# Kernel optimization log

Measured on AMD Instinct MI355X. Metric: run time of the kernel, lower is better.

The kernel has to match this reference:

```python
import jax, jax.numpy as jnp
import numpy as np

B, L, C = 8, 4096, 256
H = 8            # num_heads
D = C // H       # head_dim = 32
CHUNK = 128


def _build_slopes(n):
    # ALiBi slopes for power-of-2 n: 2^(-8/n * (i+1)); cast fp16 like the torch module
    s = np.array([2.0 ** (-(8.0 / n) * (i + 1)) for i in range(n)], dtype=np.float32)
    return jnp.asarray(s.astype(np.float16).astype(np.float32))  # [H]


def setup_inputs() -> dict:
    key = jax.random.key(0)
    ks = jax.random.split(key, 6)
    x = jax.random.normal(ks[0], (B, L, C), dtype=jnp.float32)
    rel_pos = jax.random.normal(ks[1], (1, L, C), dtype=jnp.float32) * 0.02  # trunc_normal std=0.02
    qkv_w = jax.random.normal(ks[2], (3 * C, C), dtype=jnp.float32) * (C ** -0.5)
    q_gamma = jnp.ones((H, 1, D), dtype=jnp.float32) / (D ** 0.5)
    k_gamma = jnp.ones((H, 1, D), dtype=jnp.float32) / (D ** 0.5)
    proj_w = jax.random.normal(ks[3], (C, C), dtype=jnp.float32) * (C ** -0.5)
    proj_b = jnp.zeros((C,), dtype=jnp.float32)
    return {"x": x, "rel_pos": rel_pos, "qkv_w": qkv_w, "q_gamma": q_gamma,
            "k_gamma": k_gamma, "proj_w": proj_w, "proj_b": proj_b}


def _rms_norm(t, gamma):
    # t: [B,H,L,D]; gamma: [H,1,D]. F.normalize(dim=-1) then * sqrt(D) * gamma
    n = jnp.sqrt(jnp.sum(t * t, axis=-1, keepdims=True))
    t = t / jnp.maximum(n, 1e-12)
    return t * (D ** 0.5) * gamma[None]


def _lightning_attn(q, k, v, slopes):
    # q,k,v: [B,H,L,D]; slopes: [H]. o_t = sum_{s<=t} exp(-slope*(t-s)) (q_t.k_s) v_s
    nc = L // CHUNK
    c = CHUNK
    qc = q.reshape(B, H, nc, c, D)
    kc = k.reshape(B, H, nc, c, D)
    vc = v.reshape(B, H, nc, c, D)

    idx = jnp.arange(c, dtype=jnp.float32)
    diff = idx[:, None] - idx[None, :]                       # [c,c]
    s = slopes[:, None, None]                                # [H,1,1]
    mask = jnp.where(diff >= 0, jnp.exp(-s * diff), 0.0)     # [H,c,c]

    # intra-chunk: [B,H,nc,c,c]
    scores = jnp.einsum("bhncd,bhnmd->bhncm", qc, kc) * mask[None, :, None]
    o_intra = jnp.einsum("bhncm,bhnmd->bhncd", scores, vc)

    # inter-chunk recurrence over decayed KV state [B,H,D,D]
    q_decay = jnp.exp(-slopes[:, None] * idx[None, :])[None, :, :, None]        # [1,H,c,1]
    k_decay = jnp.exp(-slopes[:, None] * (c - idx[None, :]))[None, :, :, None]  # [1,H,c,1]
    blk_decay = jnp.exp(-slopes * c)[:, None, None]                             # [H,1,1]

    def step(kv, inp):
        qi, ki, vi = inp                                   # each [B,H,c,D]
        o = jnp.einsum("bhcd,bhde->bhce", qi * q_decay, kv)
        kv = blk_decay * kv + jnp.einsum("bhcd,bhce->bhde", ki * k_decay, vi)
        return kv, o

    kv0 = jnp.zeros((B, H, D, D), dtype=q.dtype)
    qs = jnp.moveaxis(qc, 2, 0)  # [nc,B,H,c,D]
    ks_ = jnp.moveaxis(kc, 2, 0)
    vs = jnp.moveaxis(vc, 2, 0)
    _, o_inter = jax.lax.scan(step, kv0, (qs, ks_, vs))    # [nc,B,H,c,D]
    o_inter = jnp.moveaxis(o_inter, 0, 2)                  # [B,H,nc,c,D]

    return (o_intra + o_inter).reshape(B, H, L, D)


def reference(x, rel_pos, qkv_w, q_gamma, k_gamma, proj_w, proj_b):
    slopes = _build_slopes(H)
    h = x + rel_pos                                        # [B,L,C]
    qkv = h @ qkv_w.T                                      # [B,L,3C]
    qkv = qkv.reshape(B, L, 3, H, D).transpose(2, 0, 3, 1, 4)  # [3,B,H,L,D]
    q, k, v = qkv[0], qkv[1], qkv[2]
    q = q * (D ** -0.5)            # no-op through normalize, kept for fidelity
    q = _rms_norm(q, q_gamma)
    k = _rms_norm(k, k_gamma)
    o = _lightning_attn(q, k, v, slopes)                   # [B,H,L,D]
    o = o.transpose(0, 2, 1, 3).reshape(B, L, C)
    return o @ proj_w.T + proj_b
```

## Files before the change

kernel.cpp:

```cpp
#include <hip/hip_runtime.h>
#include <hip/hip_bf16.h>

#define B_ 8
#define L_ 4096
#define C_ 256
#define H_ 8
#define D_ 32
#define CHUNK_ 128
#define NC_ 32
#define M_ (B_*L_)

typedef _Float16 f16x8 __attribute__((ext_vector_type(8)));
typedef _Float16 f16x4 __attribute__((ext_vector_type(4)));
typedef float    f32x4 __attribute__((ext_vector_type(4)));

#define GLOAD_LDS16(g, l) __builtin_amdgcn_global_load_lds( \
    (const __attribute__((address_space(1))) unsigned int*)(g), \
    (__attribute__((address_space(3))) unsigned int*)(l), 16, 0, 0)

__global__ __launch_bounds__(256) void k_cast_h(
    const float* __restrict__ x, const float* __restrict__ rel, _Float16* __restrict__ h)
{
    const int i = (blockIdx.x * 256 + threadIdx.x) * 8;
    float4 x0 = *(const float4*)(x + i);
    float4 x1 = *(const float4*)(x + i + 4);
    const int ri = i & (L_ * C_ - 1);
    float4 r0 = *(const float4*)(rel + ri);
    float4 r1 = *(const float4*)(rel + ri + 4);
    f16x8 o = { (_Float16)(x0.x + r0.x), (_Float16)(x0.y + r0.y),
                (_Float16)(x0.z + r0.z), (_Float16)(x0.w + r0.w),
                (_Float16)(x1.x + r1.x), (_Float16)(x1.y + r1.y),
                (_Float16)(x1.z + r1.z), (_Float16)(x1.w + r1.w) };
    *(f16x8*)(h + i) = o;
}

__global__ __launch_bounds__(256) void k_cast_w(
    const float* __restrict__ qw, const float* __restrict__ pw,
    _Float16* __restrict__ qwb, _Float16* __restrict__ pwb)
{
    const int i = (blockIdx.x * 256 + threadIdx.x) * 4;
    const float* src; _Float16* dst; int off;
    if (i < 768 * 256) { src = qw; dst = qwb; off = i; }
    else               { src = pw; dst = pwb; off = i - 768 * 256; }
    float4 v = *(const float4*)(src + off);
    f16x4 o = { (_Float16)v.x, (_Float16)v.y, (_Float16)v.z, (_Float16)v.w };
    *(f16x4*)(dst + off) = o;
}

__global__ __launch_bounds__(256) void k_qkv_gemm(
    const _Float16* __restrict__ A, const _Float16* __restrict__ Bw,
    const float* __restrict__ qg, const float* __restrict__ kg,
    _Float16* __restrict__ Qg, _Float16* __restrict__ Kg, _Float16* __restrict__ Vtg)
{
    __shared__ __align__(16) char smem[34816];
    _Float16* As = (_Float16*)smem;
    _Float16* Bs = As + 128 * 32;
    _Float16* Ws = (_Float16*)smem;

    const int tid = threadIdx.x;
    const int wv = tid >> 6, ln = tid & 63;
    const int m0 = blockIdx.y * 128;
    const int n0 = blockIdx.x * 128;
    const int lr = ln >> 2, lc = (ln & 3) * 8;
    const int wm = (wv >> 1) * 64, wn = (wv & 1) * 64;
    const int fr = ln & 15, fk = (ln >> 4) * 8;

    f32x4 acc[4][4] = {};
    const _Float16* ga = A  + (size_t)(m0 + wv * 16 + lr) * 256 + lc;
    const _Float16* gb = Bw + (size_t)(n0 + wv * 16 + lr) * 256 + lc;

    for (int k0 = 0; k0 < 256; k0 += 32) {
        GLOAD_LDS16(ga + k0,            As + (wv * 16) * 32);
        GLOAD_LDS16(ga + k0 + 64 * 256, As + (64 + wv * 16) * 32);
        GLOAD_LDS16(gb + k0,            Bs + (wv * 16) * 32);
        GLOAD_LDS16(gb + k0 + 64 * 256, Bs + (64 + wv * 16) * 32);
        __syncthreads();
        f16x8 af[4], bf[4];
#pragma unroll
        for (int i = 0; i < 4; ++i)
            af[i] = *(const f16x8*)(As + (wm + i * 16 + fr) * 32 + fk);
#pragma unroll
        for (int j = 0; j < 4; ++j)
            bf[j] = *(const f16x8*)(Bs + (wn + j * 16 + fr) * 32 + fk);
#pragma unroll
        for (int i = 0; i < 4; ++i)
#pragma unroll
            for (int j = 0; j < 4; ++j)
                acc[i][j] = __builtin_amdgcn_mfma_f32_16x16x32_f16(
                    af[i], bf[j], acc[i][j], 0, 0, 0);
        __syncthreads();
    }

    const int cr = (ln >> 4) * 4, cc = ln & 15;
    const int kind = n0 >> 8;
    const int col0 = (n0 & 255) + wn;
    const int bb = m0 >> 12, l00 = m0 & 4095;
    const int hbase = (n0 & 255) >> 5;

    if (kind < 2) {
        const float* gsrc = kind ? kg : qg;
        float gma[2][2];
#pragma unroll
        for (int jp = 0; jp < 2; ++jp)
#pragma unroll
            for (int jj = 0; jj < 2; ++jj)
                gma[jp][jj] = gsrc[((col0 >> 5) + jp) * 32 + jj * 16 + cc];
#pragma unroll
        for (int i = 0; i < 4; ++i)
#pragma unroll
            for (int r = 0; r < 4; ++r) {
                const int irow = wm + i * 16 + cr + r;
#pragma unroll
                for (int jp = 0; jp < 2; ++jp) {
                    const float a0 = acc[i][jp * 2][r];
                    const float a1 = acc[i][jp * 2 + 1][r];
                    float ss = a0 * a0 + a1 * a1;
                    ss += __shfl_xor(ss, 1);
                    ss += __shfl_xor(ss, 2);
                    ss += __shfl_xor(ss, 4);
                    ss += __shfl_xor(ss, 8);
                    const float sc = 5.656854249492381f / fmaxf(sqrtf(ss), 1e-12f);
                    Ws[irow * 136 + wn + jp * 32 + cc]      = (_Float16)(a0 * sc * gma[jp][0]);
                    Ws[irow * 136 + wn + jp * 32 + 16 + cc] = (_Float16)(a1 * sc * gma[jp][1]);
                }
            }
        __syncthreads();
        _Float16* P = kind ? Kg : Qg;
#pragma unroll
        for (int kk = 0; kk < 8; ++kk) {
            const int c = kk * 256 + tid;
            const int hh = c >> 9;
            const int rr = (c >> 2) & 127;
            const int part = (c & 3) * 8;
            f16x8 v8 = *(const f16x8*)(Ws + rr * 136 + hh * 32 + part);
            *(f16x8*)(P + ((size_t)(bb * 8 + hbase + hh) * 4096 + l00 + rr) * 32 + part) = v8;
        }
    } else {
#pragma unroll
        for (int i = 0; i < 4; ++i)
#pragma unroll
            for (int j = 0; j < 4; ++j) {
                const int colL = wn + j * 16 + cc;
                const int row0 = wm + i * 16 + cr;
                f16x4 v4 = { (_Float16)acc[i][j][0], (_Float16)acc[i][j][1],
                             (_Float16)acc[i][j][2], (_Float16)acc[i][j][3] };
                *(f16x4*)(Ws + colL * 136 + row0) = v4;
            }
        __syncthreads();
#pragma unroll
        for (int kk = 0; kk < 8; ++kk) {
            const int q = kk * 256 + tid;
            const int c = q >> 4;
            const int seg = q & 15;
            const int col = (n0 & 255) + c;
            const int hh = col >> 5, e = col & 31;
            f16x8 v8 = *(const f16x8*)(Ws + c * 136 + seg * 8);
            *(f16x8*)(Vtg + ((size_t)(bb * 8 + hh) * 32 + e) * 4096 + l00 + seg * 8) = v8;
        }
    }
}

__global__ __launch_bounds__(256) void k_chunk_kv(
    const _Float16* __restrict__ Kg, const _Float16* __restrict__ Vtg,
    float* __restrict__ kvbuf)
{
    __shared__ float ks[128 * 32];
    __shared__ float vs[128 * 36];
    const int blk = blockIdx.x;
    const int n  = blk & 31;
    const int bh = blk >> 5;
    const int h  = bh & 7;
    const float sl2 = exp2f(-(float)(h + 1)) * 1.44269504f;
    const int tid = threadIdx.x;
    const _Float16* Kc = Kg + ((size_t)bh * 4096 + n * CHUNK_) * 32;
#pragma unroll
    for (int i = 0; i < 2; ++i) {
        const int flat = i * 256 + tid;
        const int pos = flat >> 2, d0 = (flat & 3) * 8;
        f16x8 k8 = *(const f16x8*)(Kc + flat * 8);
        const float kd = exp2f(-sl2 * (float)(CHUNK_ - pos));
        f32x4 lo = { (float)k8[0] * kd, (float)k8[1] * kd, (float)k8[2] * kd, (float)k8[3] * kd };
        f32x4 hi = { (float)k8[4] * kd, (float)k8[5] * kd, (float)k8[6] * kd, (float)k8[7] * kd };
        *(f32x4*)&ks[pos * 32 + d0]     = lo;
        *(f32x4*)&ks[pos * 32 + d0 + 4] = hi;
        const int e = flat >> 4, seg = flat & 15;
        f16x8 v8 = *(const f16x8*)(Vtg + ((size_t)bh * 32 + e) * 4096 + n * CHUNK_ + seg * 8);
#pragma unroll
        for (int j = 0; j < 8; ++j) vs[(seg * 8 + j) * 36 + e] = (float)v8[j];
    }
    __syncthreads();
    const int d = tid >> 3;
    const int e0 = (tid & 7) * 4;
    f32x4 acc = {0.f, 0.f, 0.f, 0.f};
    for (int pos = 0; pos < CHUNK_; ++pos) {
        const float kd = ks[pos * 32 + d];
        f32x4 v4 = *(const f32x4*)&vs[pos * 36 + e0];
        acc += kd * v4;
    }
    *(f32x4*)(kvbuf + (size_t)blk * 1024 + d * 32 + e0) = acc;
}

__global__ __launch_bounds__(256) void k_scan(float* __restrict__ kvbuf)
{
    const int bh = blockIdx.x;
    const int tid = threadIdx.x;
    const float slope = exp2f(-(float)((bh & 7) + 1));
    const float bd = __expf(-slope * (float)CHUNK_);
    float4 st = {0.f, 0.f, 0.f, 0.f};
    float4* base = (float4*)(kvbuf + (size_t)bh * NC_ * 1024) + tid;
#pragma unroll
    for (int g = 0; g < 4; ++g) {
        float4 tmp[8];
#pragma unroll
        for (int k = 0; k < 8; ++k) tmp[k] = base[(g * 8 + k) * 256];
#pragma unroll
        for (int k = 0; k < 8; ++k) {
            base[(g * 8 + k) * 256] = st;
            st.x = bd * st.x + tmp[k].x;
            st.y = bd * st.y + tmp[k].y;
            st.z = bd * st.z + tmp[k].z;
            st.w = bd * st.w + tmp[k].w;
        }
    }
}

__global__ __launch_bounds__(256) void k_attn(
    const _Float16* __restrict__ Qg, const _Float16* __restrict__ Kg,
    const _Float16* __restrict__ Vtg, const float* __restrict__ kvbuf,
    _Float16* __restrict__ attnp)
{
    __shared__ __align__(16) _Float16 Ss[128 * 136];
    __shared__ __align__(16) _Float16 KVt[32 * 40];
    __shared__ float ejs[CHUNK_];
    _Float16* Os = Ss;
    const int blk = blockIdx.x;
    const int n  = blk & 31;
    const int bh = blk >> 5;
    const int h  = bh & 7;
    const float sl2 = exp2f(-(float)(h + 1)) * 1.44269504f;
    const int tid = threadIdx.x;
    const int wv = tid >> 6, ln = tid & 63;
    const int fr = ln & 15, fk = (ln >> 4) * 8;
    const int cr = (ln >> 4) * 4, cc = ln & 15;

    const _Float16* Qc = Qg + ((size_t)bh * 4096 + n * CHUNK_) * 32;
    const _Float16* Kc = Kg + ((size_t)bh * 4096 + n * CHUNK_) * 32;
    const _Float16* Vc = Vtg + (size_t)bh * 32 * 4096 + n * CHUNK_;

    {
        const int e = tid & 31, dg = tid >> 5;
        const float* kvp = kvbuf + (size_t)blk * 1024;
        f16x4 kv4 = { (_Float16)kvp[(dg * 4 + 0) * 32 + e],
                      (_Float16)kvp[(dg * 4 + 1) * 32 + e],
                      (_Float16)kvp[(dg * 4 + 2) * 32 + e],
                      (_Float16)kvp[(dg * 4 + 3) * 32 + e] };
        *(f16x4*)(KVt + e * 40 + dg * 4) = kv4;
    }
    if (tid < CHUNK_) ejs[tid] = exp2f(sl2 * (float)tid);
    __syncthreads();

    f16x8 aq[2];
#pragma unroll
    for (int i = 0; i < 2; ++i)
        aq[i] = *(const f16x8*)(Qc + (wv * 32 + i * 16 + fr) * 32 + fk);

    f32x4 sacc[2][8] = {};
#pragma unroll
    for (int j = 0; j < 8; ++j) {
        f16x8 bk = *(const f16x8*)(Kc + (j * 16 + fr) * 32 + fk);
#pragma unroll
        for (int i = 0; i < 2; ++i)
            sacc[i][j] = __builtin_amdgcn_mfma_f32_16x16x32_f16(aq[i], bk, sacc[i][j], 0, 0, 0);
    }
    f32x4 iacc[2][2] = {};
#pragma unroll
    for (int ct = 0; ct < 2; ++ct) {
        f16x8 bkv = *(const f16x8*)(KVt + (ct * 16 + fr) * 40 + fk);
#pragma unroll
        for (int i = 0; i < 2; ++i)
            iacc[i][ct] = __builtin_amdgcn_mfma_f32_16x16x32_f16(aq[i], bkv, iacc[i][ct], 0, 0, 0);
    }
    float ejr[8];
#pragma unroll
    for (int j = 0; j < 8; ++j) ejr[j] = ejs[j * 16 + cc];
    const float c1 = exp2f(-sl2);
    float qd_save[2][4];
#pragma unroll
    for (int i = 0; i < 2; ++i) {
        float er = exp2f(-sl2 * (float)(wv * 32 + i * 16 + cr));
#pragma unroll
        for (int r = 0; r < 4; ++r) {
            const int irow = wv * 32 + i * 16 + cr + r;
            qd_save[i][r] = er;
#pragma unroll
            for (int j = 0; j < 8; ++j) {
                const int jcol = j * 16 + cc;
                const float w = (jcol <= irow) ? ejr[j] * er : 0.f;
                Ss[irow * 136 + jcol] = (_Float16)(sacc[i][j][r] * w);
            }
            er *= c1;
        }
    }
    __syncthreads();

    f32x4 oacc[2][2] = {};
#pragma unroll
    for (int k = 0; k < 4; ++k) {
        f16x8 as[2], bv[2];
#pragma unroll
        for (int i = 0; i < 2; ++i)
            as[i] = *(const f16x8*)(Ss + (wv * 32 + i * 16 + fr) * 136 + k * 32 + fk);
#pragma unroll
        for (int ct = 0; ct < 2; ++ct)
            bv[ct] = *(const f16x8*)(Vc + (size_t)(ct * 16 + fr) * 4096 + k * 32 + fk);
#pragma unroll
        for (int i = 0; i < 2; ++i)
#pragma unroll
            for (int ct = 0; ct < 2; ++ct)
                oacc[i][ct] = __builtin_amdgcn_mfma_f32_16x16x32_f16(as[i], bv[ct], oacc[i][ct], 0, 0, 0);
    }
    __syncthreads();
#pragma unroll
    for (int i = 0; i < 2; ++i)
#pragma unroll
        for (int r = 0; r < 4; ++r) {
            const int irow = wv * 32 + i * 16 + cr + r;
            const float qd = qd_save[i][r];
            Os[irow * 40 + cc]      = (_Float16)(oacc[i][0][r] + qd * iacc[i][0][r]);
            Os[irow * 40 + 16 + cc] = (_Float16)(oacc[i][1][r] + qd * iacc[i][1][r]);
        }
    __syncthreads();
    _Float16* abase = attnp + ((size_t)bh * 4096 + n * CHUNK_) * 32;
#pragma unroll
    for (int kk = 0; kk < 2; ++kk) {
        const int c = kk * 256 + tid;
        const int rr = c >> 2;
        const int part = (c & 3) * 8;
        *(f16x8*)(abase + rr * 32 + part) = *(const f16x8*)(Os + rr * 40 + part);
    }
}

__global__ __launch_bounds__(256) void k_proj_gemm(
    const _Float16* __restrict__ attnp, const _Float16* __restrict__ Bw,
    const float* __restrict__ bias, float* __restrict__ Cc)
{
    __shared__ _Float16 As[128 * 32];
    __shared__ _Float16 Bs[128 * 32];
    const int tid = threadIdx.x;
    const int wv = tid >> 6, ln = tid & 63;
    const int m0 = blockIdx.y * 128;
    const int n0 = blockIdx.x * 128;
    const int lr = ln >> 2;
    const int lc = (ln & 3) * 8;
    const int wm = (wv >> 1) * 64;
    const int wn = (wv & 1) * 64;
    const int fr = ln & 15;
    const int fk = (ln >> 4) * 8;

    f32x4 acc[4][4] = {};
    const int gmrow = m0 + wv * 16 + lr;
    const _Float16* ga = attnp +
        ((size_t)(gmrow >> 12) * 8 * 4096 + (gmrow & 4095)) * 32 + lc;
    const _Float16* gb = Bw + (size_t)(n0 + wv * 16 + lr) * 256 + lc;

    for (int k0 = 0; k0 < 256; k0 += 32) {
        const size_t hoff = (size_t)(k0 >> 5) * (4096 * 32);
        GLOAD_LDS16(ga + hoff,           As + (wv * 16) * 32);
        GLOAD_LDS16(ga + hoff + 64 * 32, As + (64 + wv * 16) * 32);
        GLOAD_LDS16(gb + k0,             Bs + (wv * 16) * 32);
        GLOAD_LDS16(gb + k0 + 64 * 256,  Bs + (64 + wv * 16) * 32);
        __syncthreads();
        f16x8 af[4], bf[4];
#pragma unroll
        for (int i = 0; i < 4; ++i)
            af[i] = *(const f16x8*)(As + (wm + i * 16 + fr) * 32 + fk);
#pragma unroll
        for (int j = 0; j < 4; ++j)
            bf[j] = *(const f16x8*)(Bs + (wn + j * 16 + fr) * 32 + fk);
#pragma unroll
        for (int i = 0; i < 4; ++i)
#pragma unroll
            for (int j = 0; j < 4; ++j)
                acc[i][j] = __builtin_amdgcn_mfma_f32_16x16x32_f16(
                    af[i], bf[j], acc[i][j], 0, 0, 0);
        __syncthreads();
    }
    const int cr = (ln >> 4) * 4;
    const int cc = ln & 15;
#pragma unroll
    for (int i = 0; i < 4; ++i)
#pragma unroll
        for (int j = 0; j < 4; ++j) {
            const int row = m0 + wm + i * 16 + cr;
            const int col = n0 + wn + j * 16 + cc;
            float* cp = Cc + (size_t)row * 256 + col;
            const float bb = bias[col];
#pragma unroll
            for (int r = 0; r < 4; ++r) cp[(size_t)r * 256] = acc[i][j][r] + bb;
        }
}

extern "C" void kernel_launch(void* const* d_in, const int* in_sizes, int n_in,
                              void* d_out, int out_size, void* d_ws, size_t ws_size,
                              hipStream_t stream)
{
    const float* x     = (const float*)d_in[0];
    const float* rel   = (const float*)d_in[1];
    const float* qkv_w = (const float*)d_in[2];
    const float* qg    = (const float*)d_in[3];
    const float* kg    = (const float*)d_in[4];
    const float* pw    = (const float*)d_in[5];
    const float* pb    = (const float*)d_in[6];
    float* out = (float*)d_out;
    char* wsb = (char*)d_ws;

    float*    kvb   = (float*)wsb;
    _Float16* Qg    = (_Float16*)(wsb + ((size_t)8  << 20));
    _Float16* Kg    = (_Float16*)(wsb + ((size_t)24 << 20));
    _Float16* Vtg   = (_Float16*)(wsb + ((size_t)40 << 20));
    _Float16* attnp = (_Float16*)(wsb + ((size_t)56 << 20));
    _Float16* hb    = (_Float16*)(wsb + ((size_t)72 << 20));
    _Float16* qwb   = (_Float16*)(wsb + ((size_t)88 << 20));
    _Float16* pwb   = (_Float16*)(wsb + ((size_t)89 << 20));

    k_cast_w<<<256, 256, 0, stream>>>(qkv_w, pw, qwb, pwb);
    k_cast_h<<<4096, 256, 0, stream>>>(x, rel, hb);
    k_qkv_gemm<<<dim3(6, 256), 256, 0, stream>>>(hb, qwb, qg, kg, Qg, Kg, Vtg);
    k_chunk_kv<<<2048, 256, 0, stream>>>(Kg, Vtg, kvb);
    k_scan<<<64, 256, 0, stream>>>(kvb);
    k_attn<<<2048, 256, 0, stream>>>(Qg, Kg, Vtg, kvb, attnp);
    k_proj_gemm<<<dim3(2, 256), 256, 0, stream>>>(attnp, pwb, pb, out);
}
```

Before: 188.3 us.

## Merge cast kernels, remap GEMM blocks per XCD, use MFMA for chunk KV

Merges the two cast kernels into one launch. Both GEMMs switch to a 1D grid with an XCD-aware block remap so that row tiles sharing data land on the same XCD. The per-chunk KV state kernel is rewritten as a single-wave fp16 MFMA kernel with the K decay applied in registers, replacing the fp32 scalar loop, at some cost in precision. The V-transpose LDS stride changes, and the attention kernel now reads the KV state with coalesced vector loads, which transposes how it is stored.

```diff
diff --git a/kernel.cpp b/kernel.cpp
--- a/kernel.cpp
+++ b/kernel.cpp
@@ -18,33 +18,33 @@
     (const __attribute__((address_space(1))) unsigned int*)(g), \
     (__attribute__((address_space(3))) unsigned int*)(l), 16, 0, 0)
 
-__global__ __launch_bounds__(256) void k_cast_h(
-    const float* __restrict__ x, const float* __restrict__ rel, _Float16* __restrict__ h)
-{
-    const int i = (blockIdx.x * 256 + threadIdx.x) * 8;
-    float4 x0 = *(const float4*)(x + i);
-    float4 x1 = *(const float4*)(x + i + 4);
-    const int ri = i & (L_ * C_ - 1);
-    float4 r0 = *(const float4*)(rel + ri);
-    float4 r1 = *(const float4*)(rel + ri + 4);
-    f16x8 o = { (_Float16)(x0.x + r0.x), (_Float16)(x0.y + r0.y),
-                (_Float16)(x0.z + r0.z), (_Float16)(x0.w + r0.w),
-                (_Float16)(x1.x + r1.x), (_Float16)(x1.y + r1.y),
-                (_Float16)(x1.z + r1.z), (_Float16)(x1.w + r1.w) };
-    *(f16x8*)(h + i) = o;
-}
-
-__global__ __launch_bounds__(256) void k_cast_w(
+__global__ __launch_bounds__(256) void k_prep(
+    const float* __restrict__ x, const float* __restrict__ rel,
     const float* __restrict__ qw, const float* __restrict__ pw,
-    _Float16* __restrict__ qwb, _Float16* __restrict__ pwb)
-{
-    const int i = (blockIdx.x * 256 + threadIdx.x) * 4;
-    const float* src; _Float16* dst; int off;
-    if (i < 768 * 256) { src = qw; dst = qwb; off = i; }
-    else               { src = pw; dst = pwb; off = i - 768 * 256; }
-    float4 v = *(const float4*)(src + off);
-    f16x4 o = { (_Float16)v.x, (_Float16)v.y, (_Float16)v.z, (_Float16)v.w };
-    *(f16x4*)(dst + off) = o;
+    _Float16* __restrict__ h, _Float16* __restrict__ qwb, _Float16* __restrict__ pwb)
+{
+    const int bx = blockIdx.x;
+    if (bx < 4096) {
+        const int i = (bx * 256 + threadIdx.x) * 8;
+        float4 x0 = *(const float4*)(x + i);
+        float4 x1 = *(const float4*)(x + i + 4);
+        const int ri = i & (L_ * C_ - 1);
+        float4 r0 = *(const float4*)(rel + ri);
+        float4 r1 = *(const float4*)(rel + ri + 4);
+        f16x8 o = { (_Float16)(x0.x + r0.x), (_Float16)(x0.y + r0.y),
+                    (_Float16)(x0.z + r0.z), (_Float16)(x0.w + r0.w),
+                    (_Float16)(x1.x + r1.x), (_Float16)(x1.y + r1.y),
+                    (_Float16)(x1.z + r1.z), (_Float16)(x1.w + r1.w) };
+        *(f16x8*)(h + i) = o;
+    } else {
+        const int i = ((bx - 4096) * 256 + threadIdx.x) * 4;
+        const float* src; _Float16* dst; int off;
+        if (i < 768 * 256) { src = qw; dst = qwb; off = i; }
+        else               { src = pw; dst = pwb; off = i - 768 * 256; }
+        float4 v = *(const float4*)(src + off);
+        f16x4 o = { (_Float16)v.x, (_Float16)v.y, (_Float16)v.z, (_Float16)v.w };
+        *(f16x4*)(dst + off) = o;
+    }
 }
 
 __global__ __launch_bounds__(256) void k_qkv_gemm(
@@ -57,10 +57,16 @@
     _Float16* Bs = As + 128 * 32;
     _Float16* Ws = (_Float16*)smem;
 
+    const int blk = blockIdx.x;
+    const int xcd = blk & 7;
+    const int t   = blk >> 3;
+    const int by  = xcd * 32 + (t & 31);
+    const int bx  = t >> 5;
+    const int m0 = by * 128;
+    const int n0 = bx * 128;
+
     const int tid = threadIdx.x;
     const int wv = tid >> 6, ln = tid & 63;
-    const int m0 = blockIdx.y * 128;
-    const int n0 = blockIdx.x * 128;
     const int lr = ln >> 2, lc = (ln & 3) * 8;
     const int wm = (wv >> 1) * 64, wn = (wv & 1) * 64;
     const int fr = ln & 15, fk = (ln >> 4) * 8;
@@ -144,7 +150,7 @@
                 const int row0 = wm + i * 16 + cr;
                 f16x4 v4 = { (_Float16)acc[i][j][0], (_Float16)acc[i][j][1],
                              (_Float16)acc[i][j][2], (_Float16)acc[i][j][3] };
-                *(f16x4*)(Ws + colL * 136 + row0) = v4;
+                *(f16x4*)(Ws + colL * 132 + row0) = v4;
             }
         __syncthreads();
 #pragma unroll
@@ -154,50 +160,76 @@
             const int seg = q & 15;
             const int col = (n0 & 255) + c;
             const int hh = col >> 5, e = col & 31;
-            f16x8 v8 = *(const f16x8*)(Ws + c * 136 + seg * 8);
+            f16x8 v8 = *(const f16x8*)(Ws + c * 132 + seg * 8);
             *(f16x8*)(Vtg + ((size_t)(bb * 8 + hh) * 32 + e) * 4096 + l00 + seg * 8) = v8;
         }
     }
 }
 
-__global__ __launch_bounds__(256) void k_chunk_kv(
+__global__ __launch_bounds__(64) void k_chunk_kv(
     const _Float16* __restrict__ Kg, const _Float16* __restrict__ Vtg,
     float* __restrict__ kvbuf)
 {
-    __shared__ float ks[128 * 32];
-    __shared__ float vs[128 * 36];
+    __shared__ _Float16 Vp[32 * 136];
+    __shared__ _Float16 Kp[32 * 136];
     const int blk = blockIdx.x;
     const int n  = blk & 31;
     const int bh = blk >> 5;
     const int h  = bh & 7;
     const float sl2 = exp2f(-(float)(h + 1)) * 1.44269504f;
-    const int tid = threadIdx.x;
-    const _Float16* Kc = Kg + ((size_t)bh * 4096 + n * CHUNK_) * 32;
-#pragma unroll
-    for (int i = 0; i < 2; ++i) {
-        const int flat = i * 256 + tid;
+    const int ln = threadIdx.x;
+    const _Float16* Kc = Kg  + ((size_t)bh * 4096 + n * CHUNK_) * 32;
+    const _Float16* Vc = Vtg + (size_t)bh * 32 * 4096 + n * CHUNK_;
+#pragma unroll
+    for (int i = 0; i < 8; ++i) {
+        const int flat = i * 64 + ln;
+        const int e = flat >> 4, seg = flat & 15;
+        f16x8 v8 = *(const f16x8*)(Vc + (size_t)e * 4096 + seg * 8);
+        *(f16x8*)(Vp + e * 136 + seg * 8) = v8;
         const int pos = flat >> 2, d0 = (flat & 3) * 8;
         f16x8 k8 = *(const f16x8*)(Kc + flat * 8);
-        const float kd = exp2f(-sl2 * (float)(CHUNK_ - pos));
-        f32x4 lo = { (float)k8[0] * kd, (float)k8[1] * kd, (float)k8[2] * kd, (float)k8[3] * kd };
-        f32x4 hi = { (float)k8[4] * kd, (float)k8[5] * kd, (float)k8[6] * kd, (float)k8[7] * kd };
-        *(f32x4*)&ks[pos * 32 + d0]     = lo;
-        *(f32x4*)&ks[pos * 32 + d0 + 4] = hi;
-        const int e = flat >> 4, seg = flat & 15;
-        f16x8 v8 = *(const f16x8*)(Vtg + ((size_t)bh * 32 + e) * 4096 + n * CHUNK_ + seg * 8);
-#pragma unroll
-        for (int j = 0; j < 8; ++j) vs[(seg * 8 + j) * 36 + e] = (float)v8[j];
+#pragma unroll
+        for (int j = 0; j < 8; ++j) Kp[(d0 + j) * 136 + pos] = k8[j];
     }
     __syncthreads();
-    const int d = tid >> 3;
-    const int e0 = (tid & 7) * 4;
-    f32x4 acc = {0.f, 0.f, 0.f, 0.f};
-    for (int pos = 0; pos < CHUNK_; ++pos) {
-        const float kd = ks[pos * 32 + d];
-        f32x4 v4 = *(const f32x4*)&vs[pos * 36 + e0];
-        acc += kd * v4;
-    }
-    *(f32x4*)(kvbuf + (size_t)blk * 1024 + d * 32 + e0) = acc;
+    const int fr = ln & 15, fk = (ln >> 4) * 8;
+    const float r = exp2f(sl2);
+    float rj[8];
+    rj[0] = 1.f;
+#pragma unroll
+    for (int j = 1; j < 8; ++j) rj[j] = rj[j - 1] * r;
+    f32x4 acc[2][2] = {};
+    for (int k0 = 0; k0 < 128; k0 += 32) {
+        const float e0 = exp2f(-sl2 * (float)(CHUNK_ - (k0 + fk)));
+        f16x8 av[2], bd[2];
+#pragma unroll
+        for (int i = 0; i < 2; ++i)
+            av[i] = *(const f16x8*)(Vp + (i * 16 + fr) * 136 + k0 + fk);
+#pragma unroll
+        for (int jt = 0; jt < 2; ++jt) {
+            f16x8 kraw = *(const f16x8*)(Kp + (jt * 16 + fr) * 136 + k0 + fk);
+            f16x8 kb;
+#pragma unroll
+            for (int j = 0; j < 8; ++j)
+                kb[j] = (_Float16)((float)kraw[j] * (e0 * rj[j]));
+            bd[jt] = kb;
+        }
+#pragma unroll
+        for (int i = 0; i < 2; ++i)
+#pragma unroll
+            for (int jt = 0; jt < 2; ++jt)
+                acc[i][jt] = __builtin_amdgcn_mfma_f32_16x16x32_f16(
+                    av[i], bd[jt], acc[i][jt], 0, 0, 0);
+    }
+    const int cr = (ln >> 4) * 4, cc = ln & 15;
+    float* outp = kvbuf + (size_t)blk * 1024;
+#pragma unroll
+    for (int i = 0; i < 2; ++i)
+#pragma unroll
+        for (int jt = 0; jt < 2; ++jt)
+#pragma unroll
+            for (int rr = 0; rr < 4; ++rr)
+                outp[(i * 16 + cr + rr) * 32 + jt * 16 + cc] = acc[i][jt][rr];
 }
 
 __global__ __launch_bounds__(256) void k_scan(float* __restrict__ kvbuf)
@@ -248,13 +280,11 @@
     const _Float16* Vc = Vtg + (size_t)bh * 32 * 4096 + n * CHUNK_;
 
     {
-        const int e = tid & 31, dg = tid >> 5;
         const float* kvp = kvbuf + (size_t)blk * 1024;
-        f16x4 kv4 = { (_Float16)kvp[(dg * 4 + 0) * 32 + e],
-                      (_Float16)kvp[(dg * 4 + 1) * 32 + e],
-                      (_Float16)kvp[(dg * 4 + 2) * 32 + e],
-                      (_Float16)kvp[(dg * 4 + 3) * 32 + e] };
-        *(f16x4*)(KVt + e * 40 + dg * 4) = kv4;
+        f32x4 kv4f = *(const f32x4*)(kvp + tid * 4);
+        f16x4 kv4 = { (_Float16)kv4f[0], (_Float16)kv4f[1],
+                      (_Float16)kv4f[2], (_Float16)kv4f[3] };
+        *(f16x4*)(KVt + (tid >> 3) * 40 + (tid & 7) * 4) = kv4;
     }
     if (tid < CHUNK_) ejs[tid] = exp2f(sl2 * (float)tid);
     __syncthreads();
@@ -346,10 +376,14 @@
 {
     __shared__ _Float16 As[128 * 32];
     __shared__ _Float16 Bs[128 * 32];
+    const int blk = blockIdx.x;
+    const int xcd = blk & 7;
+    const int t   = blk >> 3;
+    const int m0 = (xcd * 32 + (t & 31)) * 128;
+    const int n0 = (t >> 5) * 128;
+
     const int tid = threadIdx.x;
     const int wv = tid >> 6, ln = tid & 63;
-    const int m0 = blockIdx.y * 128;
-    const int n0 = blockIdx.x * 128;
     const int lr = ln >> 2;
     const int lc = (ln & 3) * 8;
     const int wm = (wv >> 1) * 64;
@@ -423,11 +457,10 @@
     _Float16* qwb   = (_Float16*)(wsb + ((size_t)88 << 20));
     _Float16* pwb   = (_Float16*)(wsb + ((size_t)89 << 20));
 
-    k_cast_w<<<256, 256, 0, stream>>>(qkv_w, pw, qwb, pwb);
-    k_cast_h<<<4096, 256, 0, stream>>>(x, rel, hb);
-    k_qkv_gemm<<<dim3(6, 256), 256, 0, stream>>>(hb, qwb, qg, kg, Qg, Kg, Vtg);
-    k_chunk_kv<<<2048, 256, 0, stream>>>(Kg, Vtg, kvb);
+    k_prep<<<4352, 256, 0, stream>>>(x, rel, qkv_w, pw, hb, qwb, pwb);
+    k_qkv_gemm<<<1536, 256, 0, stream>>>(hb, qwb, qg, kg, Qg, Kg, Vtg);
+    k_chunk_kv<<<2048, 64, 0, stream>>>(Kg, Vtg, kvb);
     k_scan<<<64, 256, 0, stream>>>(kvb);
     k_attn<<<2048, 256, 0, stream>>>(Qg, Kg, Vtg, kvb, attnp);
-    k_proj_gemm<<<dim3(2, 256), 256, 0, stream>>>(attnp, pwb, pb, out);
-}
+    k_proj_gemm<<<512, 256, 0, stream>>>(attnp, pwb, pb, out);
+}
```

New measurement: 168.2 us. 1.12x faster.
